# Kernel tuning notes

Measured on AMD Instinct MI355X. Metric: run time of the kernel, lower is better.

## Reference

```python
import jax, jax.numpy as jnp
import numpy as np


def postorder_positions(depth):
    """Post-order index of each node in a perfect binary tree of given depth.
    Returns dict: level -> np.array of post-order indices for the left-to-right
    nodes at that level (level 0 = leaves, level `depth` = root)."""
    levels = {0: np.array([0], dtype=np.int64)}
    size = 1  # size of depth-(d-1) subtree
    for d in range(1, depth + 1):
        new = {l: np.concatenate([levels[l], levels[l] + size]) for l in range(d)}
        new[d] = np.array([2 * size], dtype=np.int64)
        levels = new
        size = 2 * size + 1
    return levels


def setup_inputs() -> dict:
    key = jax.random.key(0)
    k1, k2, k3, k4, k5, k6 = jax.random.split(key, 6)
    VOCAB, E, LBL, LEAVES = 50000, 100, 2, 131072  # 2**17 leaves
    word_ids = jax.random.randint(k1, (LEAVES,), 0, VOCAB, dtype=jnp.int32)
    emb_table = jax.random.normal(k2, (VOCAB, E), dtype=jnp.float32) * 0.1
    Wl = jax.random.normal(k3, (E, E), dtype=jnp.float32) * 0.1
    bl = jax.random.normal(k4, (E,), dtype=jnp.float32) * 0.1
    Wp = jax.random.normal(k5, (LBL, E), dtype=jnp.float32) * 0.1
    bp = jax.random.normal(k6, (LBL,), dtype=jnp.float32) * 0.1
    return {"word_ids": word_ids, "emb_table": emb_table, "Wl": Wl, "bl": bl, "Wp": Wp, "bp": bp}


def reference(word_ids, emb_table, Wl, bl, Wp, bp):
    # Perfect binary tree, batched level-by-level (same math as the per-node
    # Python recursion in the torch module). NOTE: original uses fcl for BOTH
    # children, so internal node = relu(fcl(left) + fcl(right)).
    L = word_ids.shape[0]
    D = int(round(np.log2(L)))
    pos = postorder_positions(D)
    n_nodes = 2 * L - 1

    h = emb_table[word_ids]  # [L, E] leaf states
    out = jnp.zeros((n_nodes, 1, bp.shape[0]), dtype=h.dtype)
    for lvl in range(D + 1):
        proj = h @ Wp.T + bp                     # [n_lvl, label]
        out = out.at[jnp.asarray(pos[lvl])].set(proj[:, None, :])
        if lvl < D:
            # fcl(left)+fcl(right) = (left+right) @ Wl^T + 2*bl, then relu
            h = jax.nn.relu((h[0::2] + h[1::2]) @ Wl.T + 2.0 * bl)
    return out  # [n_nodes, 1, label] in post-order, matching torch.cat(node_list)
```

## Files before the change

### kernel.cpp

```cpp
#include <hip/hip_runtime.h>

typedef _Float16 h8v __attribute__((ext_vector_type(8)));
typedef float f4v __attribute__((ext_vector_type(4)));

#define RS 136
#define SD 68

__device__ __forceinline__ unsigned pk2f(float a, float b) {
  unsigned short ha = __builtin_bit_cast(unsigned short, (_Float16)a);
  unsigned short hb = __builtin_bit_cast(unsigned short, (_Float16)b);
  return (unsigned)ha | ((unsigned)hb << 16);
}
__device__ __forceinline__ float2 upk(unsigned u) {
  _Float16 lo = __builtin_bit_cast(_Float16, (unsigned short)(u & 0xffffu));
  _Float16 hi = __builtin_bit_cast(_Float16, (unsigned short)(u >> 16));
  return make_float2((float)lo, (float)hi);
}

__global__ void prep_kernel(const float* __restrict__ Wl,
                            unsigned short* __restrict__ Wlf) {
  int i = blockIdx.x * 256 + threadIdx.x;
  if (i < 128 * 128) {
    int o = i >> 7, k = i & 127;
    _Float16 v = (_Float16)0.f;
    if (o < 100 && k < 100) v = (_Float16)Wl[o * 100 + k];
    Wlf[i] = __builtin_bit_cast(unsigned short, v);
  }
}

__device__ __forceinline__ void load_bfrags(
    const unsigned short* __restrict__ Wlf, const float* __restrict__ bl,
    h8v (&B0)[4], h8v (&B1)[4], float& bias0, float& bias1,
    int wave, int quad, int c16) {
  int col0 = wave * 32 + c16;
  int col1 = col0 + 16;
  bias0 = (col0 < 100) ? 2.0f * bl[col0] : 0.f;
  bias1 = (col1 < 100) ? 2.0f * bl[col1] : 0.f;
  const _Float16* w0 = (const _Float16*)Wlf + col0 * 128 + quad * 8;
  const _Float16* w1 = (const _Float16*)Wlf + col1 * 128 + quad * 8;
  B0[0] = *(const h8v*)(w0);      B0[1] = *(const h8v*)(w0 + 32);
  B0[2] = *(const h8v*)(w0 + 64); B0[3] = *(const h8v*)(w0 + 96);
  B1[0] = *(const h8v*)(w1);      B1[1] = *(const h8v*)(w1 + 32);
  B1[2] = *(const h8v*)(w1 + 64); B1[3] = *(const h8v*)(w1 + 96);
}

__device__ __forceinline__ void mfma_level(
    const _Float16* srcE, const _Float16* srcO, bool pairMode,
    _Float16* dstE, _Float16* dstO, int nOut,
    const h8v (&B0)[4], const h8v (&B1)[4], float bias0, float bias1,
    int lane, int wave) {
  const int quad = lane >> 4, c16 = lane & 15;
  const int col0 = wave * 32 + c16, col1 = col0 + 16;
  const int tiles = (nOut + 15) >> 4;
  for (int rt = 0; rt < tiles; ++rt) {
    const int r = rt * 16 + c16;
    const h8v* pe = (const h8v*)(srcE + (size_t)r * RS + quad * 8);
    h8v A0, A1, A2, A3;
    if (pairMode) {
      const h8v* po = (const h8v*)(srcO + (size_t)r * RS + quad * 8);
      A0 = pe[0] + po[0];  A1 = pe[4] + po[4];
      A2 = pe[8] + po[8];  A3 = pe[12] + po[12];
    } else {
      A0 = pe[0]; A1 = pe[4]; A2 = pe[8]; A3 = pe[12];
    }
    f4v a0 = {bias0, bias0, bias0, bias0};
    f4v a1 = {bias1, bias1, bias1, bias1};
    a0 = __builtin_amdgcn_mfma_f32_16x16x32_f16(A0, B0[0], a0, 0, 0, 0);
    a0 = __builtin_amdgcn_mfma_f32_16x16x32_f16(A1, B0[1], a0, 0, 0, 0);
    a0 = __builtin_amdgcn_mfma_f32_16x16x32_f16(A2, B0[2], a0, 0, 0, 0);
    a0 = __builtin_amdgcn_mfma_f32_16x16x32_f16(A3, B0[3], a0, 0, 0, 0);
    a1 = __builtin_amdgcn_mfma_f32_16x16x32_f16(A0, B1[0], a1, 0, 0, 0);
    a1 = __builtin_amdgcn_mfma_f32_16x16x32_f16(A1, B1[1], a1, 0, 0, 0);
    a1 = __builtin_amdgcn_mfma_f32_16x16x32_f16(A2, B1[2], a1, 0, 0, 0);
    a1 = __builtin_amdgcn_mfma_f32_16x16x32_f16(A3, B1[3], a1, 0, 0, 0);
    #pragma unroll
    for (int rg = 0; rg < 4; ++rg) {
      int row = rt * 16 + quad * 4 + rg;
      _Float16* dr = ((row & 1) ? dstO : dstE) + (size_t)(row >> 1) * RS;
      dr[col0] = (_Float16)fmaxf(a0[rg], 0.f);
      dr[col1] = (_Float16)fmaxf(a1[rg], 0.f);
    }
  }
}

__device__ __forceinline__ void proj_rows(
    const _Float16* E, const _Float16* O, int nRows, const float* WpS,
    float bp0, float bp1, int lvl, long gbase, float* __restrict__ out, int tid) {
  if (tid >= nRows) return;
  const unsigned* row = (const unsigned*)((tid & 1) ? O : E) + (size_t)(tid >> 1) * SD;
  float q0 = bp0, q1 = bp1;
  #pragma unroll
  for (int p = 0; p < 25; ++p) {
    uint2 u = ((const uint2*)row)[p];
    float2 a = upk(u.x), b = upk(u.y);
    q0 = fmaf(a.x, WpS[4*p], fmaf(a.y, WpS[4*p+1],
         fmaf(b.x, WpS[4*p+2], fmaf(b.y, WpS[4*p+3], q0))));
    q1 = fmaf(a.x, WpS[100+4*p], fmaf(a.y, WpS[100+4*p+1],
         fmaf(b.x, WpS[100+4*p+2], fmaf(b.y, WpS[100+4*p+3], q1))));
  }
  long g = gbase + tid;
  long pos = ((g + 1) << (lvl + 1)) - 2 - __popc((unsigned)g);
  out[2 * pos] = q0; out[2 * pos + 1] = q1;
}

__global__ __launch_bounds__(256, 3) void leaf_kernel(
    const int* __restrict__ word_ids, const float* __restrict__ emb,
    const unsigned short* __restrict__ Wlf, const float* __restrict__ bl,
    const float* __restrict__ Wp, const float* __restrict__ bp,
    unsigned* __restrict__ h7g, float* __restrict__ out) {
  __shared__ _Float16 S1[64 * RS];
  __shared__ _Float16 Ea[32 * RS], Oa[32 * RS];
  __shared__ _Float16 Eb[16 * RS], Ob[16 * RS];
  __shared__ float WpS[200];
  const int tid = threadIdx.x, lane = tid & 63;
  const int wave = __builtin_amdgcn_readfirstlane(tid >> 6);
  const int quad = lane >> 4, c16 = lane & 15;
  const int blk = blockIdx.x;

  if (tid < 200) WpS[tid] = Wp[tid];
  {
    unsigned* S1d = (unsigned*)S1;
    for (int i = tid; i < 64 * 14; i += 256) S1d[(i / 14) * SD + 50 + (i % 14)] = 0;
  }
  const float bp0 = bp[0], bp1 = bp[1];

  const int l = tid >> 1, hh = tid & 1;
  const long gL = (long)blk * 128 + l;
  const float4* row4 = (const float4*)(emb + (size_t)word_ids[gL] * 100);
  float4 v[13];
  #pragma unroll
  for (int i = 0; i < 13; ++i) {
    int q = 13 * hh + i;
    if (q < 25) v[i] = row4[q];
  }
  __syncthreads();

  {
    float q0 = 0.f, q1 = 0.f;
    #pragma unroll
    for (int i = 0; i < 13; ++i) {
      int q = 13 * hh + i;
      if (q < 25) {
        q0 = fmaf(v[i].x, WpS[4*q], fmaf(v[i].y, WpS[4*q+1],
             fmaf(v[i].z, WpS[4*q+2], fmaf(v[i].w, WpS[4*q+3], q0))));
        q1 = fmaf(v[i].x, WpS[100+4*q], fmaf(v[i].y, WpS[100+4*q+1],
             fmaf(v[i].z, WpS[100+4*q+2], fmaf(v[i].w, WpS[100+4*q+3], q1))));
      }
    }
    q0 += __shfl_xor(q0, 1, 64);
    q1 += __shfl_xor(q1, 1, 64);
    if (hh == 0) {
      long pos = ((gL + 1) << 1) - 2 - __popc((unsigned)gL);
      out[2 * pos] = q0 + bp0; out[2 * pos + 1] = q1 + bp1;
    }
  }
  {
    unsigned* S1d = (unsigned*)S1;
    #pragma unroll
    for (int i = 0; i < 13; ++i) {
      int q = 13 * hh + i;
      if (q < 25) {
        float sx = v[i].x + __shfl_xor(v[i].x, 2, 64);
        float sy = v[i].y + __shfl_xor(v[i].y, 2, 64);
        float sz = v[i].z + __shfl_xor(v[i].z, 2, 64);
        float sw = v[i].w + __shfl_xor(v[i].w, 2, 64);
        if ((tid & 2) == 0) {
          int m = tid >> 2;
          S1d[m * SD + 2*q]     = pk2f(sx, sy);
          S1d[m * SD + 2*q + 1] = pk2f(sz, sw);
        }
      }
    }
  }
  h8v B0[4], B1[4]; float bias0, bias1;
  load_bfrags(Wlf, bl, B0, B1, bias0, bias1, wave, quad, c16);
  __syncthreads();

  mfma_level(S1, nullptr, false, Ea, Oa, 64, B0, B1, bias0, bias1, lane, wave);
  __syncthreads();
  mfma_level(Ea, Oa, true, Eb, Ob, 32, B0, B1, bias0, bias1, lane, wave);
  proj_rows(Ea, Oa, 64, WpS, bp0, bp1, 1, (long)blk * 64, out, tid);
  __syncthreads();
  mfma_level(Eb, Ob, true, Ea, Oa, 16, B0, B1, bias0, bias1, lane, wave);
  proj_rows(Eb, Ob, 32, WpS, bp0, bp1, 2, (long)blk * 32, out, tid);
  __syncthreads();
  mfma_level(Ea, Oa, true, Eb, Ob, 8, B0, B1, bias0, bias1, lane, wave);
  proj_rows(Ea, Oa, 16, WpS, bp0, bp1, 3, (long)blk * 16, out, tid);
  __syncthreads();
  mfma_level(Eb, Ob, true, Ea, Oa, 4, B0, B1, bias0, bias1, lane, wave);
  proj_rows(Eb, Ob, 8, WpS, bp0, bp1, 4, (long)blk * 8, out, tid);
  __syncthreads();
  mfma_level(Ea, Oa, true, Eb, Ob, 2, B0, B1, bias0, bias1, lane, wave);
  proj_rows(Ea, Oa, 4, WpS, bp0, bp1, 5, (long)blk * 4, out, tid);
  __syncthreads();
  mfma_level(Eb, Ob, true, Ea, Oa, 1, B0, B1, bias0, bias1, lane, wave);
  proj_rows(Eb, Ob, 2, WpS, bp0, bp1, 6, (long)blk * 2, out, tid);
  __syncthreads();
  if (tid < 50) h7g[(size_t)blk * 50 + tid] = ((unsigned*)Ea)[tid];
}

__global__ __launch_bounds__(256) void tree_kernel(
    const unsigned* __restrict__ hsrc, unsigned* __restrict__ hdst,
    const unsigned short* __restrict__ Wlf, const float* __restrict__ bl,
    const float* __restrict__ Wp, const float* __restrict__ bp,
    float* __restrict__ out, int firstLvl, int nLvl, int nIn, int finalProj) {
  __shared__ _Float16 Ea[32 * RS], Oa[32 * RS];
  __shared__ _Float16 Eb[16 * RS], Ob[16 * RS];
  __shared__ float WpS[200];
  const int tid = threadIdx.x, lane = tid & 63;
  const int wave = __builtin_amdgcn_readfirstlane(tid >> 6);
  const int quad = lane >> 4, c16 = lane & 15;
  const int blk = blockIdx.x;

  if (tid < 200) WpS[tid] = Wp[tid];
  const float bp0 = bp[0], bp1 = bp[1];

  {
    const unsigned* src = hsrc + (size_t)blk * nIn * 50;
    unsigned* Ed = (unsigned*)Ea; unsigned* Od = (unsigned*)Oa;
    for (int i = tid; i < 64 * 64; i += 256) {
      int r = i >> 6, d = i & 63;
      unsigned val = (r < nIn && d < 50) ? src[(size_t)r * 50 + d] : 0u;
      ((r & 1) ? Od : Ed)[(r >> 1) * SD + d] = val;
    }
    unsigned* Ed2 = (unsigned*)Eb; unsigned* Od2 = (unsigned*)Ob;
    for (int i = tid; i < 32 * 64; i += 256) {
      int r = i >> 6, d = i & 63;
      ((r & 1) ? Od2 : Ed2)[(r >> 1) * SD + d] = 0u;
    }
  }
  h8v B0[4], B1[4]; float bias0, bias1;
  load_bfrags(Wlf, bl, B0, B1, bias0, bias1, wave, quad, c16);
  __syncthreads();

  _Float16 *sE = Ea, *sO = Oa, *dE = Eb, *dO = Ob;
  int n = nIn >> 1;
  for (int p = 0; p < nLvl; ++p) {
    mfma_level(sE, sO, true, dE, dO, n, B0, B1, bias0, bias1, lane, wave);
    proj_rows(sE, sO, n * 2, WpS, bp0, bp1, firstLvl + p - 1,
              (long)blk * (n * 2), out, tid);
    __syncthreads();
    _Float16* t;
    t = sE; sE = dE; dE = t;
    t = sO; sO = dO; dO = t;
    n >>= 1;
  }
  int R = nIn >> nLvl;
  if (finalProj)
    proj_rows(sE, sO, R, WpS, bp0, bp1, firstLvl + nLvl - 1, (long)blk * R, out, tid);
  if (hdst) {
    for (int i = tid; i < R * 50; i += 256) {
      int r = i / 50, d = i % 50;
      hdst[(size_t)blk * R * 50 + i] =
          ((const unsigned*)((r & 1) ? sO : sE))[(r >> 1) * SD + d];
    }
  }
}

extern "C" void kernel_launch(void* const* d_in, const int* in_sizes, int n_in,
                              void* d_out, int out_size, void* d_ws, size_t ws_size,
                              hipStream_t stream) {
  const int*   word_ids = (const int*)  d_in[0];
  const float* emb      = (const float*)d_in[1];
  const float* Wl       = (const float*)d_in[2];
  const float* bl       = (const float*)d_in[3];
  const float* Wp       = (const float*)d_in[4];
  const float* bp       = (const float*)d_in[5];
  float* out = (float*)d_out;

  unsigned short* Wlf = (unsigned short*)d_ws;
  unsigned* h7g  = (unsigned*)((char*)d_ws + 32768);
  unsigned* h13g = (unsigned*)((char*)d_ws + 32768 + 204800);

  prep_kernel<<<64, 256, 0, stream>>>(Wl, Wlf);
  leaf_kernel<<<1024, 256, 0, stream>>>(word_ids, emb, Wlf, bl, Wp, bp, h7g, out);
  tree_kernel<<<16, 256, 0, stream>>>(h7g, h13g, Wlf, bl, Wp, bp, out, 8, 6, 64, 0);
  tree_kernel<<<1, 256, 0, stream>>>(h13g, nullptr, Wlf, bl, Wp, bp, out, 14, 4, 16, 1);
}
```

Baseline: 152.8 us.

## Fuse leaf and tree kernels into one with last-block-done atomic counters

Merges the prep, leaf and two tree kernels into a single launch. The last block of each 64-block group (found with an atomic counter) runs the middle tree levels, and the last of those runs the top levels. The separate Wl fp16 conversion kernel is dropped in favour of each thread converting its own B fragments from fp32 Wl. LDS is trimmed by aliasing Eb/Ob onto S1 and occupancy is raised to 4, aiming to remove launch gaps and tail serialization, at the cost of a memset, extra scalar global loads per block and serial tail work inside one block.

```diff
diff --git a/kernel.cpp b/kernel.cpp
--- a/kernel.cpp
+++ b/kernel.cpp
@@ -17,31 +17,25 @@
   return make_float2((float)lo, (float)hi);
 }
 
-__global__ void prep_kernel(const float* __restrict__ Wl,
-                            unsigned short* __restrict__ Wlf) {
-  int i = blockIdx.x * 256 + threadIdx.x;
-  if (i < 128 * 128) {
-    int o = i >> 7, k = i & 127;
-    _Float16 v = (_Float16)0.f;
-    if (o < 100 && k < 100) v = (_Float16)Wl[o * 100 + k];
-    Wlf[i] = __builtin_bit_cast(unsigned short, v);
-  }
-}
-
-__device__ __forceinline__ void load_bfrags(
-    const unsigned short* __restrict__ Wlf, const float* __restrict__ bl,
+__device__ __forceinline__ void make_bfrags(
+    const float* __restrict__ Wl, const float* __restrict__ bl,
     h8v (&B0)[4], h8v (&B1)[4], float& bias0, float& bias1,
     int wave, int quad, int c16) {
-  int col0 = wave * 32 + c16;
-  int col1 = col0 + 16;
+  const int col0 = wave * 32 + c16, col1 = col0 + 16;
   bias0 = (col0 < 100) ? 2.0f * bl[col0] : 0.f;
   bias1 = (col1 < 100) ? 2.0f * bl[col1] : 0.f;
-  const _Float16* w0 = (const _Float16*)Wlf + col0 * 128 + quad * 8;
-  const _Float16* w1 = (const _Float16*)Wlf + col1 * 128 + quad * 8;
-  B0[0] = *(const h8v*)(w0);      B0[1] = *(const h8v*)(w0 + 32);
-  B0[2] = *(const h8v*)(w0 + 64); B0[3] = *(const h8v*)(w0 + 96);
-  B1[0] = *(const h8v*)(w1);      B1[1] = *(const h8v*)(w1 + 32);
-  B1[2] = *(const h8v*)(w1 + 64); B1[3] = *(const h8v*)(w1 + 96);
+  #pragma unroll
+  for (int j = 0; j < 4; ++j) {
+    const int k0 = quad * 8 + j * 32;
+    #pragma unroll
+    for (int m = 0; m < 8; ++m) {
+      const int k = k0 + m;
+      float w0 = (col0 < 100 && k < 100) ? Wl[col0 * 100 + k] : 0.f;
+      float w1 = (col1 < 100 && k < 100) ? Wl[col1 * 100 + k] : 0.f;
+      B0[j][m] = (_Float16)w0;
+      B1[j][m] = (_Float16)w1;
+    }
+  }
 }
 
 __device__ __forceinline__ void mfma_level(
@@ -103,15 +97,65 @@
   out[2 * pos] = q0; out[2 * pos + 1] = q1;
 }
 
-__global__ __launch_bounds__(256, 3) void leaf_kernel(
+__device__ void tree_phase(
+    const unsigned* __restrict__ src, unsigned* __restrict__ hdst,
+    _Float16* Ea, _Float16* Oa, _Float16* Eb, _Float16* Ob,
+    const float* WpS, float bp0, float bp1,
+    const h8v (&B0)[4], const h8v (&B1)[4], float bias0, float bias1,
+    float* __restrict__ out, int firstLvl, int nLvl, int nIn, int finalProj,
+    long blk, int tid, int lane, int wave) {
+  {
+    unsigned* Ed = (unsigned*)Ea; unsigned* Od = (unsigned*)Oa;
+    for (int i = tid; i < 64 * 64; i += 256) {
+      int r = i >> 6, d = i & 63;
+      unsigned val = (r < nIn && d < 50) ? src[(size_t)r * 50 + d] : 0u;
+      ((r & 1) ? Od : Ed)[(r >> 1) * SD + d] = val;
+    }
+    unsigned* Ed2 = (unsigned*)Eb; unsigned* Od2 = (unsigned*)Ob;
+    for (int i = tid; i < 32 * 64; i += 256) {
+      int r = i >> 6, d = i & 63;
+      ((r & 1) ? Od2 : Ed2)[(r >> 1) * SD + d] = 0u;
+    }
+  }
+  __syncthreads();
+  _Float16 *sE = Ea, *sO = Oa, *dE = Eb, *dO = Ob;
+  int n = nIn >> 1;
+  for (int p = 0; p < nLvl; ++p) {
+    mfma_level(sE, sO, true, dE, dO, n, B0, B1, bias0, bias1, lane, wave);
+    proj_rows(sE, sO, n * 2, WpS, bp0, bp1, firstLvl + p - 1,
+              blk * (n * 2), out, tid);
+    __syncthreads();
+    _Float16* t;
+    t = sE; sE = dE; dE = t;
+    t = sO; sO = dO; dO = t;
+    n >>= 1;
+  }
+  int R = nIn >> nLvl;
+  if (finalProj)
+    proj_rows(sE, sO, R, WpS, bp0, bp1, firstLvl + nLvl - 1, blk * R, out, tid);
+  if (hdst) {
+    for (int i = tid; i < R * 50; i += 256) {
+      int r = i / 50, d = i % 50;
+      hdst[(size_t)blk * R * 50 + i] =
+          ((const unsigned*)((r & 1) ? sO : sE))[(r >> 1) * SD + d];
+    }
+  }
+  __syncthreads();
+}
+
+__global__ __launch_bounds__(256, 4) void mega_kernel(
     const int* __restrict__ word_ids, const float* __restrict__ emb,
-    const unsigned short* __restrict__ Wlf, const float* __restrict__ bl,
+    const float* __restrict__ Wl, const float* __restrict__ bl,
     const float* __restrict__ Wp, const float* __restrict__ bp,
-    unsigned* __restrict__ h7g, float* __restrict__ out) {
+    unsigned* __restrict__ h7g, unsigned* __restrict__ h13g,
+    unsigned* __restrict__ cnts, float* __restrict__ out) {
   __shared__ _Float16 S1[64 * RS];
   __shared__ _Float16 Ea[32 * RS], Oa[32 * RS];
-  __shared__ _Float16 Eb[16 * RS], Ob[16 * RS];
   __shared__ float WpS[200];
+  __shared__ int claimS;
+  _Float16* const Eb = S1;
+  _Float16* const Ob = S1 + 16 * RS;
+
   const int tid = threadIdx.x, lane = tid & 63;
   const int wave = __builtin_amdgcn_readfirstlane(tid >> 6);
   const int quad = lane >> 4, c16 = lane & 15;
@@ -173,7 +217,7 @@
     }
   }
   h8v B0[4], B1[4]; float bias0, bias1;
-  load_bfrags(Wlf, bl, B0, B1, bias0, bias1, wave, quad, c16);
+  make_bfrags(Wl, bl, B0, B1, bias0, bias1, wave, quad, c16);
   __syncthreads();
 
   mfma_level(S1, nullptr, false, Ea, Oa, 64, B0, B1, bias0, bias1, lane, wave);
@@ -197,64 +241,34 @@
   proj_rows(Eb, Ob, 2, WpS, bp0, bp1, 6, (long)blk * 2, out, tid);
   __syncthreads();
   if (tid < 50) h7g[(size_t)blk * 50 + tid] = ((unsigned*)Ea)[tid];
-}
-
-__global__ __launch_bounds__(256) void tree_kernel(
-    const unsigned* __restrict__ hsrc, unsigned* __restrict__ hdst,
-    const unsigned short* __restrict__ Wlf, const float* __restrict__ bl,
-    const float* __restrict__ Wp, const float* __restrict__ bp,
-    float* __restrict__ out, int firstLvl, int nLvl, int nIn, int finalProj) {
-  __shared__ _Float16 Ea[32 * RS], Oa[32 * RS];
-  __shared__ _Float16 Eb[16 * RS], Ob[16 * RS];
-  __shared__ float WpS[200];
-  const int tid = threadIdx.x, lane = tid & 63;
-  const int wave = __builtin_amdgcn_readfirstlane(tid >> 6);
-  const int quad = lane >> 4, c16 = lane & 15;
-  const int blk = blockIdx.x;
-
-  if (tid < 200) WpS[tid] = Wp[tid];
-  const float bp0 = bp[0], bp1 = bp[1];
-
-  {
-    const unsigned* src = hsrc + (size_t)blk * nIn * 50;
-    unsigned* Ed = (unsigned*)Ea; unsigned* Od = (unsigned*)Oa;
-    for (int i = tid; i < 64 * 64; i += 256) {
-      int r = i >> 6, d = i & 63;
-      unsigned val = (r < nIn && d < 50) ? src[(size_t)r * 50 + d] : 0u;
-      ((r & 1) ? Od : Ed)[(r >> 1) * SD + d] = val;
-    }
-    unsigned* Ed2 = (unsigned*)Eb; unsigned* Od2 = (unsigned*)Ob;
-    for (int i = tid; i < 32 * 64; i += 256) {
-      int r = i >> 6, d = i & 63;
-      ((r & 1) ? Od2 : Ed2)[(r >> 1) * SD + d] = 0u;
-    }
-  }
-  h8v B0[4], B1[4]; float bias0, bias1;
-  load_bfrags(Wlf, bl, B0, B1, bias0, bias1, wave, quad, c16);
-  __syncthreads();
-
-  _Float16 *sE = Ea, *sO = Oa, *dE = Eb, *dO = Ob;
-  int n = nIn >> 1;
-  for (int p = 0; p < nLvl; ++p) {
-    mfma_level(sE, sO, true, dE, dO, n, B0, B1, bias0, bias1, lane, wave);
-    proj_rows(sE, sO, n * 2, WpS, bp0, bp1, firstLvl + p - 1,
-              (long)blk * (n * 2), out, tid);
-    __syncthreads();
-    _Float16* t;
-    t = sE; sE = dE; dE = t;
-    t = sO; sO = dO; dO = t;
-    n >>= 1;
-  }
-  int R = nIn >> nLvl;
-  if (finalProj)
-    proj_rows(sE, sO, R, WpS, bp0, bp1, firstLvl + nLvl - 1, (long)blk * R, out, tid);
-  if (hdst) {
-    for (int i = tid; i < R * 50; i += 256) {
-      int r = i / 50, d = i % 50;
-      hdst[(size_t)blk * R * 50 + i] =
-          ((const unsigned*)((r & 1) ? sO : sE))[(r >> 1) * SD + d];
-    }
-  }
+  __syncthreads();
+
+  const int g = blk >> 6;
+  if (tid == 0) {
+    __threadfence();
+    unsigned old = atomicAdd(&cnts[g], 1u);
+    int c = (old == 63u);
+    if (c) __threadfence();
+    claimS = c;
+  }
+  __syncthreads();
+  if (!claimS) return;
+
+  tree_phase(h7g + (size_t)g * 64 * 50, h13g, Ea, Oa, Eb, Ob, WpS, bp0, bp1,
+             B0, B1, bias0, bias1, out, 8, 6, 64, 0, (long)g, tid, lane, wave);
+
+  if (tid == 0) {
+    __threadfence();
+    unsigned old = atomicAdd(&cnts[16], 1u);
+    int c = (old == 15u);
+    if (c) __threadfence();
+    claimS = c;
+  }
+  __syncthreads();
+  if (!claimS) return;
+
+  tree_phase(h13g, nullptr, Ea, Oa, Eb, Ob, WpS, bp0, bp1,
+             B0, B1, bias0, bias1, out, 14, 4, 16, 1, 0L, tid, lane, wave);
 }
 
 extern "C" void kernel_launch(void* const* d_in, const int* in_sizes, int n_in,
@@ -268,12 +282,11 @@
   const float* bp       = (const float*)d_in[5];
   float* out = (float*)d_out;
 
-  unsigned short* Wlf = (unsigned short*)d_ws;
-  unsigned* h7g  = (unsigned*)((char*)d_ws + 32768);
-  unsigned* h13g = (unsigned*)((char*)d_ws + 32768 + 204800);
-
-  prep_kernel<<<64, 256, 0, stream>>>(Wl, Wlf);
-  leaf_kernel<<<1024, 256, 0, stream>>>(word_ids, emb, Wlf, bl, Wp, bp, h7g, out);
-  tree_kernel<<<16, 256, 0, stream>>>(h7g, h13g, Wlf, bl, Wp, bp, out, 8, 6, 64, 0);
-  tree_kernel<<<1, 256, 0, stream>>>(h13g, nullptr, Wlf, bl, Wp, bp, out, 14, 4, 16, 1);
-}
+  unsigned* h7g  = (unsigned*)d_ws;
+  unsigned* h13g = (unsigned*)((char*)d_ws + 204800);
+  unsigned* cnts = (unsigned*)((char*)d_ws + 208000);
+
+  hipMemsetAsync(cnts, 0, 128, stream);
+  mega_kernel<<<1024, 256, 0, stream>>>(word_ids, emb, Wl, bl, Wp, bp,
+                                        h7g, h13g, cnts, out);
+}
```

Result: slower. 168.0 us (+10.0%).
